# Kernel optimization log

Measured on AMD Instinct MI355X. Metric: run time of the kernel, lower is better.

The kernel has to match this reference:

```python
import jax, jax.numpy as jnp
import numpy as np

N = 50000      # nodes per type (tx and addr)
E = 400000     # edges per relation
IN, H, OUT = 128, 256, 2
RELS = ['tt', 'aa', 'at', 'ta']


def setup_inputs() -> dict:
    key = jax.random.key(0)
    ks = jax.random.split(key, 32)
    inp = {}
    inp['x_tx'] = jax.random.normal(ks[0], (N, IN), jnp.float32)
    inp['x_addr'] = jax.random.normal(ks[1], (N, IN), jnp.float32)
    for i, r in enumerate(RELS):
        inp['e_' + r] = jax.random.randint(ks[2 + i], (2, E), 0, N, jnp.int32)
    k = 6
    for li, (din, dout) in enumerate([(IN, H), (H, OUT)]):
        for r in RELS:
            inp[f'Wl{li}_{r}'] = jax.random.normal(ks[k], (dout, din), jnp.float32) * 0.05; k += 1
            inp[f'bl{li}_{r}'] = jnp.zeros((dout,), jnp.float32)
            inp[f'Wr{li}_{r}'] = jax.random.normal(ks[k], (dout, din), jnp.float32) * 0.05; k += 1
    return inp


def _sage(x_src, x_dst, edge, Wl, bl, Wr):
    # PyG SAGEConv: lin_l(mean_{j in N(i)} x_j) + lin_r(x_i)
    n = x_dst.shape[0]
    msg = x_src[edge[0]]                                         # [E, d] gather
    s = jax.ops.segment_sum(msg, edge[1], num_segments=n)        # [n, d] scatter-add
    cnt = jax.ops.segment_sum(jnp.ones((edge.shape[1],), x_src.dtype), edge[1], num_segments=n)
    agg = s / jnp.maximum(cnt, 1.0)[:, None]                     # mean (0 for isolated)
    return agg @ Wl.T + bl + x_dst @ Wr.T


def reference(x_tx, x_addr, e_tt, e_aa, e_at, e_ta,
              Wl0_tt, bl0_tt, Wr0_tt, Wl0_aa, bl0_aa, Wr0_aa,
              Wl0_at, bl0_at, Wr0_at, Wl0_ta, bl0_ta, Wr0_ta,
              Wl1_tt, bl1_tt, Wr1_tt, Wl1_aa, bl1_aa, Wr1_aa,
              Wl1_at, bl1_at, Wr1_at, Wl1_ta, bl1_ta, Wr1_ta):
    # Layer 0: HeteroConv with aggr='sum' over relations per destination type
    h_tx = _sage(x_tx, x_tx, e_tt, Wl0_tt, bl0_tt, Wr0_tt) + \
           _sage(x_addr, x_tx, e_at, Wl0_at, bl0_at, Wr0_at)
    h_ad = _sage(x_addr, x_addr, e_aa, Wl0_aa, bl0_aa, Wr0_aa) + \
           _sage(x_tx, x_addr, e_ta, Wl0_ta, bl0_ta, Wr0_ta)
    h_tx = jax.nn.relu(h_tx)   # dropout is identity at inference
    h_ad = jax.nn.relu(h_ad)
    # Layer 1 (output)
    o_tx = _sage(h_tx, h_tx, e_tt, Wl1_tt, bl1_tt, Wr1_tt) + \
           _sage(h_ad, h_tx, e_at, Wl1_at, bl1_at, Wr1_at)
    o_ad = _sage(h_ad, h_ad, e_aa, Wl1_aa, bl1_aa, Wr1_aa) + \
           _sage(h_tx, h_ad, e_ta, Wl1_ta, bl1_ta, Wr1_ta)
    return o_tx, o_ad
```

## Files before the change

kernel.cpp:

```cpp
#include <hip/hip_runtime.h>
#include <hip/hip_fp8.h>


#define DIN 128
#define DH  256
#define LDSA 136
#define LDSH 264

typedef __attribute__((ext_vector_type(8))) short bf16x8;
typedef __attribute__((ext_vector_type(4))) float f32x4;
typedef __attribute__((ext_vector_type(2))) float f32x2;

__device__ __forceinline__ float blo(unsigned u) { return __uint_as_float(u << 16); }
__device__ __forceinline__ float bhi(unsigned u) { return __uint_as_float(u & 0xffff0000u); }
__device__ __forceinline__ unsigned short f2bf(float f) {
    unsigned int u = __float_as_uint(f);
    u = (u + 0x7fffu + ((u >> 16) & 1u)) >> 16;
    return (unsigned short)u;
}

#if __has_builtin(__builtin_amdgcn_cvt_pk_fp8_f32) && __has_builtin(__builtin_amdgcn_cvt_pk_f32_fp8)
__device__ __forceinline__ unsigned pk_fp8(float4 a) {
    unsigned v = (unsigned)__builtin_amdgcn_cvt_pk_fp8_f32(a.x, a.y, 0, false);
    v = (unsigned)__builtin_amdgcn_cvt_pk_fp8_f32(a.z, a.w, (int)v, true);
    return v;
}
__device__ __forceinline__ void acc_fp8x4(float* a, unsigned u) {
    f32x2 f0 = __builtin_amdgcn_cvt_pk_f32_fp8((int)u, false);
    f32x2 f1 = __builtin_amdgcn_cvt_pk_f32_fp8((int)u, true);
    a[0] += f0.x; a[1] += f0.y; a[2] += f1.x; a[3] += f1.y;
}
#else
__device__ __forceinline__ unsigned pk_fp8(float4 a) {
    __hip_fp8_e4m3 v0(a.x), v1(a.y), v2(a.z), v3(a.w);
    return (unsigned)v0.__x | ((unsigned)v1.__x << 8) |
           ((unsigned)v2.__x << 16) | ((unsigned)v3.__x << 24);
}
__device__ __forceinline__ void acc_fp8x4(float* a, unsigned u) {
    __hip_fp8_e4m3 v0, v1, v2, v3;
    v0.__x = (unsigned char)(u & 0xff);
    v1.__x = (unsigned char)((u >> 8) & 0xff);
    v2.__x = (unsigned char)((u >> 16) & 0xff);
    v3.__x = (unsigned char)((u >> 24) & 0xff);
    a[0] += (float)v0; a[1] += (float)v1; a[2] += (float)v2; a[3] += (float)v3;
}
#endif

__device__ __forceinline__ void acc_fp8x16(float* a, uint4 u) {
    acc_fp8x4(a + 0,  u.x);
    acc_fp8x4(a + 4,  u.y);
    acc_fp8x4(a + 8,  u.z);
    acc_fp8x4(a + 12, u.w);
}

__global__ __launch_bounds__(256) void setup_kernel(
    const float* __restrict__ x_tx, const float* __restrict__ x_addr,
    const float* __restrict__ Wl0_tt, const float* __restrict__ Wl0_aa,
    const float* __restrict__ Wl0_at, const float* __restrict__ Wl0_ta,
    const float* __restrict__ Wr0_tt, const float* __restrict__ Wr0_aa,
    const float* __restrict__ Wr0_at, const float* __restrict__ Wr0_ta,
    const float* __restrict__ bl0_tt, const float* __restrict__ bl0_aa,
    const float* __restrict__ bl0_at, const float* __restrict__ bl0_ta,
    const float* __restrict__ Wl1_tt, const float* __restrict__ Wl1_aa,
    const float* __restrict__ Wl1_at, const float* __restrict__ Wl1_ta,
    const float* __restrict__ Wr1_tt, const float* __restrict__ Wr1_aa,
    const float* __restrict__ Wr1_at, const float* __restrict__ Wr1_ta,
    const float* __restrict__ bl1_tt, const float* __restrict__ bl1_aa,
    const float* __restrict__ bl1_at, const float* __restrict__ bl1_ta,
    unsigned short* __restrict__ xb_tx, unsigned short* __restrict__ xb_ad,
    uint2* __restrict__ x8_tx, uint2* __restrict__ x8_ad,
    unsigned short* __restrict__ wb_tt, unsigned short* __restrict__ wb_aa,
    unsigned short* __restrict__ wb_at, unsigned short* __restrict__ wb_ta,
    unsigned short* __restrict__ wr0c_tx, unsigned short* __restrict__ wr0c_ad,
    float* __restrict__ b0c, unsigned short* __restrict__ wzb,
    float* __restrict__ b1c, int N)
{
    int i = blockIdx.x * blockDim.x + threadIdx.x;
    int nconv = N * DIN / 8;
    if (i < nconv) {
        {
            const float4* p = (const float4*)(x_tx + (size_t)i * 8);
            float4 a = p[0], b = p[1];
            uint4 o;
            o.x = (unsigned)f2bf(a.x) | ((unsigned)f2bf(a.y) << 16);
            o.y = (unsigned)f2bf(a.z) | ((unsigned)f2bf(a.w) << 16);
            o.z = (unsigned)f2bf(b.x) | ((unsigned)f2bf(b.y) << 16);
            o.w = (unsigned)f2bf(b.z) | ((unsigned)f2bf(b.w) << 16);
            *(uint4*)(xb_tx + (size_t)i * 8) = o;
            x8_tx[i] = make_uint2(pk_fp8(a), pk_fp8(b));
        }
        {
            const float4* p = (const float4*)(x_addr + (size_t)i * 8);
            float4 a = p[0], b = p[1];
            uint4 o;
            o.x = (unsigned)f2bf(a.x) | ((unsigned)f2bf(a.y) << 16);
            o.y = (unsigned)f2bf(a.z) | ((unsigned)f2bf(a.w) << 16);
            o.z = (unsigned)f2bf(b.x) | ((unsigned)f2bf(b.y) << 16);
            o.w = (unsigned)f2bf(b.z) | ((unsigned)f2bf(b.w) << 16);
            *(uint4*)(xb_ad + (size_t)i * 8) = o;
            x8_ad[i] = make_uint2(pk_fp8(a), pk_fp8(b));
        }
    }
    if (i < DH * DIN) {
        wb_tt[i] = f2bf(Wl0_tt[i]);
        wb_aa[i] = f2bf(Wl0_aa[i]);
        wb_at[i] = f2bf(Wl0_at[i]);
        wb_ta[i] = f2bf(Wl0_ta[i]);
        wr0c_tx[i] = f2bf(Wr0_tt[i] + Wr0_at[i]);
        wr0c_ad[i] = f2bf(Wr0_aa[i] + Wr0_ta[i]);
    }
    if (i < DH) {
        b0c[i]      = bl0_tt[i] + bl0_at[i];
        b0c[DH + i] = bl0_aa[i] + bl0_ta[i];
    }
    if (i < 2 * 16 * DH) {
        int type = i >> 12;
        int rem = i & 4095;
        int r = rem >> 8;
        int c = rem & 255;
        float v = 0.f;
        if (r < 6) {
            const float* A = type ? Wl1_aa : Wl1_tt;
            const float* B = type ? Wl1_at : Wl1_ta;
            if (r == 0) v = A[c];
            else if (r == 1) v = A[DH + c];
            else if (r == 2) v = B[c];
            else if (r == 3) v = B[DH + c];
            else if (r == 4) v = type ? (Wr1_aa[c] + Wr1_ta[c]) : (Wr1_tt[c] + Wr1_at[c]);
            else             v = type ? (Wr1_aa[DH + c] + Wr1_ta[DH + c])
                                      : (Wr1_tt[DH + c] + Wr1_at[DH + c]);
        }
        wzb[i] = f2bf(v);
    }
    if (i < 2) {
        b1c[i]     = bl1_tt[i] + bl1_at[i];
        b1c[2 + i] = bl1_aa[i] + bl1_ta[i];
    }
}

__global__ __launch_bounds__(256) void count_kernel(
    const int* __restrict__ e0, const int* __restrict__ e1,
    const int* __restrict__ e2, const int* __restrict__ e3,
    int* __restrict__ cnt, int* __restrict__ rank, int E, int N)
{
    int r = blockIdx.y;
    const int* e = (r == 0) ? e0 : (r == 1) ? e1 : (r == 2) ? e2 : e3;
    int base = (blockIdx.x * 256 + threadIdx.x) * 8;
    int* cb = cnt + r * N;
    int* rk = rank + (size_t)r * E;
    if (base + 8 <= E) {
        int4 d0 = *(const int4*)(e + E + base);
        int4 d1 = *(const int4*)(e + E + base + 4);
        int4 r0, r1;
        r0.x = atomicAdd(&cb[d0.x], 1);
        r0.y = atomicAdd(&cb[d0.y], 1);
        r0.z = atomicAdd(&cb[d0.z], 1);
        r0.w = atomicAdd(&cb[d0.w], 1);
        r1.x = atomicAdd(&cb[d1.x], 1);
        r1.y = atomicAdd(&cb[d1.y], 1);
        r1.z = atomicAdd(&cb[d1.z], 1);
        r1.w = atomicAdd(&cb[d1.w], 1);
        *(int4*)(rk + base) = r0;
        *(int4*)(rk + base + 4) = r1;
    } else {
        for (int i = base; i < E; ++i)
            rk[i] = atomicAdd(&cb[e[E + i]], 1);
    }
}

__global__ __launch_bounds__(1024) void scan_kernel(
    const int* __restrict__ cnt, int* __restrict__ excl,
    unsigned long long* __restrict__ desc, int n)
{
    __shared__ int sdata[1024];
    __shared__ int sseg;
    __shared__ int sprev;
    if (threadIdx.x == 0) sseg = (int)atomicAdd(&desc[256], 1ULL);
    __syncthreads();
    int seg = sseg;
    int i = seg * 1024 + threadIdx.x;
    int v = (i < n) ? cnt[i] : 0;
    sdata[threadIdx.x] = v;
    __syncthreads();
    for (int off = 1; off < 1024; off <<= 1) {
        int t = (threadIdx.x >= off) ? sdata[threadIdx.x - off] : 0;
        __syncthreads();
        sdata[threadIdx.x] += t;
        __syncthreads();
    }
    if (threadIdx.x == 0) {
        int total = sdata[1023];
        int prev = 0;
        if (seg == 0) {
            atomicExch(&desc[0], ((unsigned long long)(unsigned)total << 2) | 2ULL);
        } else {
            atomicExch(&desc[seg], ((unsigned long long)(unsigned)total << 2) | 1ULL);
            int j = seg - 1;
            for (;;) {
                unsigned long long d = atomicAdd(&desc[j], 0ULL);
                unsigned st = (unsigned)(d & 3ULL);
                if (st == 0u) continue;
                prev += (int)(d >> 2);
                if (st == 2u) break;
                --j;
            }
            atomicExch(&desc[seg],
                       ((unsigned long long)(unsigned)(prev + total) << 2) | 2ULL);
        }
        sprev = prev;
    }
    __syncthreads();
    if (i < n) excl[i] = sprev + sdata[threadIdx.x] - v;
}

__global__ __launch_bounds__(256) void fill_kernel(
    const int* __restrict__ e0, const int* __restrict__ e1,
    const int* __restrict__ e2, const int* __restrict__ e3,
    const int* __restrict__ rowptr, const int* __restrict__ rank,
    int* __restrict__ col, int E, int N)
{
    int r = blockIdx.y;
    const int* e = (r == 0) ? e0 : (r == 1) ? e1 : (r == 2) ? e2 : e3;
    const int* rp = rowptr + r * N;
    const int* rk = rank + (size_t)r * E;
    int base = (blockIdx.x * 256 + threadIdx.x) * 4;
    if (base + 4 <= E) {
        int4 s = *(const int4*)(e + base);
        int4 d = *(const int4*)(e + E + base);
        int4 rr = *(const int4*)(rk + base);
        int p0 = rp[d.x], p1 = rp[d.y], p2 = rp[d.z], p3 = rp[d.w];
        col[p0 + rr.x] = s.x;
        col[p1 + rr.y] = s.y;
        col[p2 + rr.z] = s.z;
        col[p3 + rr.w] = s.w;
    } else {
        for (int i = base; i < E; ++i)
            col[rp[e[E + i]] + rk[i]] = e[i];
    }
}

__global__ __launch_bounds__(256) void agg_kernel(
    const uint4* __restrict__ x8_tx, const uint4* __restrict__ x8_ad,
    const int* __restrict__ rowptr, const int* __restrict__ cnt,
    const int* __restrict__ col, unsigned short* __restrict__ aggb, int N)
{
    int r = blockIdx.y;
    const uint4* xs = (r == 0 || r == 3) ? x8_tx : x8_ad;
    int t = threadIdx.x;
    int wv = t >> 6;
    int l  = t & 63;
    int oct = l >> 3;
    int d   = l & 7;
    int node = blockIdx.x * 32 + wv * 8 + oct;
    if (node >= N) return;
    int idx = r * N + node;
    int base = rowptr[idx];
    int c    = cnt[idx];
    const int* cl = col + base;
    float a0[16] = {}, a1[16] = {};
    int e = 0;
    for (; e + 2 <= c; e += 2) {
        int s0 = cl[e];
        int s1 = cl[e + 1];
        uint4 u0 = xs[((unsigned)s0 << 3) + d];
        uint4 u1 = xs[((unsigned)s1 << 3) + d];
        acc_fp8x16(a0, u0);
        acc_fp8x16(a1, u1);
    }
    if (e < c) {
        int s0 = cl[e];
        uint4 u0 = xs[((unsigned)s0 << 3) + d];
        acc_fp8x16(a0, u0);
    }
    float sc = 1.0f / fmaxf((float)c, 1.0f);
    uint4 o0, o1;
    o0.x = (unsigned)f2bf((a0[0] + a1[0]) * sc)  | ((unsigned)f2bf((a0[1] + a1[1]) * sc) << 16);
    o0.y = (unsigned)f2bf((a0[2] + a1[2]) * sc)  | ((unsigned)f2bf((a0[3] + a1[3]) * sc) << 16);
    o0.z = (unsigned)f2bf((a0[4] + a1[4]) * sc)  | ((unsigned)f2bf((a0[5] + a1[5]) * sc) << 16);
    o0.w = (unsigned)f2bf((a0[6] + a1[6]) * sc)  | ((unsigned)f2bf((a0[7] + a1[7]) * sc) << 16);
    o1.x = (unsigned)f2bf((a0[8] + a1[8]) * sc)  | ((unsigned)f2bf((a0[9] + a1[9]) * sc) << 16);
    o1.y = (unsigned)f2bf((a0[10] + a1[10]) * sc) | ((unsigned)f2bf((a0[11] + a1[11]) * sc) << 16);
    o1.z = (unsigned)f2bf((a0[12] + a1[12]) * sc) | ((unsigned)f2bf((a0[13] + a1[13]) * sc) << 16);
    o1.w = (unsigned)f2bf((a0[14] + a1[14]) * sc) | ((unsigned)f2bf((a0[15] + a1[15]) * sc) << 16);
    uint4* orow = (uint4*)(aggb + ((size_t)r * N + node) * DIN);
    orow[d * 2]     = o0;
    orow[d * 2 + 1] = o1;
}

__global__ __launch_bounds__(256) void gemm0z_kernel(
    const unsigned short* __restrict__ xb_tx, const unsigned short* __restrict__ xb_ad,
    const unsigned short* __restrict__ aggb,
    const unsigned short* __restrict__ wb_tt, const unsigned short* __restrict__ wb_at,
    const unsigned short* __restrict__ wr0c_tx,
    const unsigned short* __restrict__ wb_aa, const unsigned short* __restrict__ wb_ta,
    const unsigned short* __restrict__ wr0c_ad,
    const float* __restrict__ b0c, const unsigned short* __restrict__ wzb,
    const float* __restrict__ b1c,
    float* __restrict__ z, float* __restrict__ outp, int N)
{
    __shared__ unsigned short lds[3 * 64 * LDSA];
    const int type = blockIdx.y;
    const unsigned short* xself = type ? xb_ad : xb_tx;
    const unsigned short* A0 = aggb + (size_t)(type ? 1 : 0) * N * DIN;
    const unsigned short* A1 = aggb + (size_t)(type ? 3 : 2) * N * DIN;
    const unsigned short* W0 = type ? wb_aa   : wb_tt;
    const unsigned short* W1 = type ? wb_ta   : wb_at;
    const unsigned short* W2 = type ? wr0c_ad : wr0c_tx;
    const float* bias = b0c + type * DH;
    float* zA = type ? (z + (size_t)1 * N * 2) : z;
    float* zB = type ? (z + (size_t)2 * N * 2) : (z + (size_t)3 * N * 2);
    float* outSelf = outp + (size_t)type * N * 2;

    const int t  = threadIdx.x;
    const int wv = t >> 6;
    const int l  = t & 63;
    const int q  = l >> 4;
    const int lr = l & 15;
    const int m0 = blockIdx.x * 64;
    const int n0 = wv * 64;

    {
        const uint4* As[3] = {(const uint4*)A0, (const uint4*)A1, (const uint4*)xself};
#pragma unroll
        for (int i = 0; i < 12; ++i) {
            int cid = i * 256 + t;
            int seg = cid >> 10;
            int rem = cid & 1023;
            int row = rem >> 4;
            int ch  = rem & 15;
            int gr = m0 + row; if (gr >= N) gr = N - 1;
            uint4 v = As[seg][((unsigned)gr << 4) + ch];
            *(uint4*)&lds[(seg * 64 + row) * LDSA + ch * 8] = v;
        }
    }
    __syncthreads();

    f32x4 accm[4][4] = {};
    {
        const unsigned short* Ws[3] = {W0, W1, W2};
        for (int seg = 0; seg < 3; ++seg) {
            const unsigned short* W = Ws[seg];
            const unsigned short* la = &lds[(seg * 64 + lr) * LDSA + q * 8];
            const unsigned short* pb0 = W + (unsigned)(n0 + lr) * DIN + q * 8;
            const unsigned short* pb1 = W + (unsigned)(n0 + 16 + lr) * DIN + q * 8;
            const unsigned short* pb2 = W + (unsigned)(n0 + 32 + lr) * DIN + q * 8;
            const unsigned short* pb3 = W + (unsigned)(n0 + 48 + lr) * DIN + q * 8;
#pragma unroll
            for (int k = 0; k < DIN; k += 32) {
                bf16x8 b0 = *(const bf16x8*)(pb0 + k);
                bf16x8 b1 = *(const bf16x8*)(pb1 + k);
                bf16x8 b2 = *(const bf16x8*)(pb2 + k);
                bf16x8 b3 = *(const bf16x8*)(pb3 + k);
#pragma unroll
                for (int mt = 0; mt < 4; ++mt) {
                    bf16x8 a = *(const bf16x8*)(la + mt * 16 * LDSA + k);
                    accm[mt][0] = __builtin_amdgcn_mfma_f32_16x16x32_bf16(a, b0, accm[mt][0], 0, 0, 0);
                    accm[mt][1] = __builtin_amdgcn_mfma_f32_16x16x32_bf16(a, b1, accm[mt][1], 0, 0, 0);
                    accm[mt][2] = __builtin_amdgcn_mfma_f32_16x16x32_bf16(a, b2, accm[mt][2], 0, 0, 0);
                    accm[mt][3] = __builtin_amdgcn_mfma_f32_16x16x32_bf16(a, b3, accm[mt][3], 0, 0, 0);
                }
            }
        }
    }
    __syncthreads();

    {
        float bias_nt[4];
#pragma unroll
        for (int nt = 0; nt < 4; ++nt) bias_nt[nt] = bias[n0 + nt * 16 + lr];
#pragma unroll
        for (int mt = 0; mt < 4; ++mt) {
#pragma unroll
            for (int nt = 0; nt < 4; ++nt) {
                int colc = n0 + nt * 16 + lr;
#pragma unroll
                for (int rr = 0; rr < 4; ++rr) {
                    int row = mt * 16 + q * 4 + rr;
                    lds[row * LDSH + colc] =
                        f2bf(fmaxf(accm[mt][nt][rr] + bias_nt[nt], 0.f));
                }
            }
        }
    }
    __syncthreads();

    {
        const unsigned short* wz = wzb + (size_t)type * 16 * DH;
        f32x4 az = {};
        const unsigned short* la = &lds[(wv * 16 + lr) * LDSH + q * 8];
        const unsigned short* pb = wz + lr * DH + q * 8;
#pragma unroll
        for (int k = 0; k < DH; k += 32) {
            bf16x8 a = *(const bf16x8*)(la + k);
            bf16x8 b = *(const bf16x8*)(pb + k);
            az = __builtin_amdgcn_mfma_f32_16x16x32_bf16(a, b, az, 0, 0, 0);
        }
        if (lr < 6) {
#pragma unroll
            for (int reg = 0; reg < 4; ++reg) {
                int node = m0 + wv * 16 + q * 4 + reg;
                if (node < N) {
                    float v = az[reg];
                    if (lr < 2)      zA[node * 2 + lr] = v;
                    else if (lr < 4) zB[node * 2 + lr - 2] = v;
                    else             outSelf[node * 2 + lr - 4] = v + b1c[type * 2 + lr - 4];
                }
            }
        }
    }
}

__global__ __launch_bounds__(256) void l1_agg_kernel(
    const int* __restrict__ rowptr, const int* __restrict__ cnt, const int* __restrict__ col,
    const float* __restrict__ z, float* __restrict__ out, int N)
{
    const int type = blockIdx.y;
    const int rA = type ? 1 : 0;
    const int rB = type ? 3 : 2;
    const float* zAp = type ? (z + (size_t)1 * N * 2) : z;
    const float* zBp = type ? (z + (size_t)3 * N * 2) : (z + (size_t)2 * N * 2);
    float* outp = out + (size_t)type * N * 2;

    const int t = threadIdx.x;
    const int wave = t >> 6;
    const int l = t & 63;
    const int sub = l >> 3;
    const int es  = l & 7;
    int node = blockIdx.x * 32 + wave * 8 + sub;
    bool valid = node < N;

    float ax = 0.f, ay = 0.f;
#pragma unroll
    for (int ri = 0; ri < 2; ++ri) {
        int rel = ri ? rB : rA;
        const float* zp = ri ? zBp : zAp;
        int b = 0, c = 0;
        if (valid) { b = rowptr[rel * N + node]; c = cnt[rel * N + node]; }
        const int* cl = col + b;
        float sx = 0.f, sy = 0.f;
        for (int e = es; e < c; e += 8) {
            int s = cl[e];
            float2 v = *(const float2*)(zp + (size_t)s * 2);
            sx += v.x; sy += v.y;
        }
        sx += __shfl_xor(sx, 1, 64); sy += __shfl_xor(sy, 1, 64);
        sx += __shfl_xor(sx, 2, 64); sy += __shfl_xor(sy, 2, 64);
        sx += __shfl_xor(sx, 4, 64); sy += __shfl_xor(sy, 4, 64);
        float sc = 1.0f / fmaxf((float)c, 1.0f);
        ax += sx * sc; ay += sy * sc;
    }
    if (valid && es == 0) {
        float2 o = *(float2*)(outp + (size_t)node * 2);
        o.x += ax; o.y += ay;
        *(float2*)(outp + (size_t)node * 2) = o;
    }
}

extern "C" void kernel_launch(void* const* d_in, const int* in_sizes, int n_in,
                              void* d_out, int out_size, void* d_ws, size_t ws_size,
                              hipStream_t stream)
{
    const float* x_tx   = (const float*)d_in[0];
    const float* x_addr = (const float*)d_in[1];
    const int* e_tt = (const int*)d_in[2];
    const int* e_aa = (const int*)d_in[3];
    const int* e_at = (const int*)d_in[4];
    const int* e_ta = (const int*)d_in[5];
    const float* Wl0_tt = (const float*)d_in[6];
    const float* bl0_tt = (const float*)d_in[7];
    const float* Wr0_tt = (const float*)d_in[8];
    const float* Wl0_aa = (const float*)d_in[9];
    const float* bl0_aa = (const float*)d_in[10];
    const float* Wr0_aa = (const float*)d_in[11];
    const float* Wl0_at = (const float*)d_in[12];
    const float* bl0_at = (const float*)d_in[13];
    const float* Wr0_at = (const float*)d_in[14];
    const float* Wl0_ta = (const float*)d_in[15];
    const float* bl0_ta = (const float*)d_in[16];
    const float* Wr0_ta = (const float*)d_in[17];
    const float* Wl1_tt = (const float*)d_in[18];
    const float* bl1_tt = (const float*)d_in[19];
    const float* Wr1_tt = (const float*)d_in[20];
    const float* Wl1_aa = (const float*)d_in[21];
    const float* bl1_aa = (const float*)d_in[22];
    const float* Wr1_aa = (const float*)d_in[23];
    const float* Wl1_at = (const float*)d_in[24];
    const float* bl1_at = (const float*)d_in[25];
    const float* Wr1_at = (const float*)d_in[26];
    const float* Wl1_ta = (const float*)d_in[27];
    const float* bl1_ta = (const float*)d_in[28];
    const float* Wr1_ta = (const float*)d_in[29];

    const int N = in_sizes[0] / DIN;
    const int E = in_sizes[2] / 2;

    size_t off = 0;
    char* base = (char*)d_ws;
    auto alloc = [&](size_t bytes) -> void* {
        void* p = base + off;
        off += (bytes + 255) & ~(size_t)255;
        return p;
    };
    int*   cnt    = (int*)  alloc((size_t)4 * N * 4);
    unsigned long long* desc = (unsigned long long*)alloc(257 * 8);
    int*   rowptr = (int*)  alloc((size_t)4 * N * 4);
    int*   rank   = (int*)  alloc((size_t)4 * E * 4);
    int*   col    = (int*)  alloc((size_t)4 * E * 4);
    unsigned short* xb_tx = (unsigned short*)alloc((size_t)N * DIN * 2);
    unsigned short* xb_ad = (unsigned short*)alloc((size_t)N * DIN * 2);
    uint2* x8_tx = (uint2*)alloc((size_t)N * DIN);
    uint2* x8_ad = (uint2*)alloc((size_t)N * DIN);
    unsigned short* aggb  = (unsigned short*)alloc((size_t)4 * N * DIN * 2);
    float* z      = (float*)alloc((size_t)4 * N * 2 * 4);
    unsigned short* wb_tt  = (unsigned short*)alloc((size_t)DH * DIN * 2);
    unsigned short* wb_aa  = (unsigned short*)alloc((size_t)DH * DIN * 2);
    unsigned short* wb_at  = (unsigned short*)alloc((size_t)DH * DIN * 2);
    unsigned short* wb_ta  = (unsigned short*)alloc((size_t)DH * DIN * 2);
    unsigned short* wr0c_tx = (unsigned short*)alloc((size_t)DH * DIN * 2);
    unsigned short* wr0c_ad = (unsigned short*)alloc((size_t)DH * DIN * 2);
    float* b0c    = (float*)alloc((size_t)2 * DH * 4);
    unsigned short* wzb = (unsigned short*)alloc((size_t)2 * 16 * DH * 2);
    float* b1c    = (float*)alloc((size_t)2 * 2 * 4);
    (void)ws_size;

    float* outp = (float*)d_out;
    const int n4 = 4 * N;

    hipMemsetAsync(cnt, 0, (((size_t)4 * N * 4 + 255) & ~(size_t)255) + 257 * 8, stream);

    {
        int nconv = N * DIN / 8;
        setup_kernel<<<(nconv + 255) / 256, 256, 0, stream>>>(
            x_tx, x_addr,
            Wl0_tt, Wl0_aa, Wl0_at, Wl0_ta,
            Wr0_tt, Wr0_aa, Wr0_at, Wr0_ta,
            bl0_tt, bl0_aa, bl0_at, bl0_ta,
            Wl1_tt, Wl1_aa, Wl1_at, Wl1_ta,
            Wr1_tt, Wr1_aa, Wr1_at, Wr1_ta,
            bl1_tt, bl1_aa, bl1_at, bl1_ta,
            xb_tx, xb_ad, x8_tx, x8_ad,
            wb_tt, wb_aa, wb_at, wb_ta, wr0c_tx, wr0c_ad,
            b0c, wzb, b1c, N);
    }
    {
        dim3 g((E + 2047) / 2048, 4);
        count_kernel<<<g, 256, 0, stream>>>(e_tt, e_aa, e_at, e_ta, cnt, rank, E, N);
    }
    {
        int nb = (n4 + 1023) / 1024;
        scan_kernel<<<nb, 1024, 0, stream>>>(cnt, rowptr, desc, n4);
    }
    {
        dim3 g((E + 1023) / 1024, 4);
        fill_kernel<<<g, 256, 0, stream>>>(e_tt, e_aa, e_at, e_ta, rowptr, rank, col, E, N);
    }
    {
        dim3 g((N + 31) / 32, 4);
        agg_kernel<<<g, 256, 0, stream>>>((const uint4*)x8_tx, (const uint4*)x8_ad,
                                          rowptr, cnt, col, aggb, N);
    }
    {
        dim3 g((N + 63) / 64, 2);
        gemm0z_kernel<<<g, 256, 0, stream>>>(
            xb_tx, xb_ad, aggb,
            wb_tt, wb_at, wr0c_tx, wb_aa, wb_ta, wr0c_ad,
            b0c, wzb, b1c, z, outp, N);
    }
    {
        dim3 g((N + 31) / 32, 2);
        l1_agg_kernel<<<g, 256, 0, stream>>>(rowptr, cnt, col, z, outp, N);
    }
}
```

Baseline: 375.3 us.

## Build CSR via two-level bucket sort with LDS histograms instead of global atomics

Replaces the per-edge global atomic counting, decoupled-lookback scan and random fill with a two-pass bucket sort. Edges are first grouped into coarse buckets of 256 destinations using shared-memory histograms and one global atomic per bucket per block. A per-bucket kernel then sorts within the bucket in LDS and writes rowptr, cnt and col. This cuts global atomic contention and random scattered writes. The costs are an extra temp buffer pass, source ids packed into 16 bits (valid only for N ≤ 65536), and non-deterministic edge order within a row.

```diff
diff --git a/kernel.cpp b/kernel.cpp
--- a/kernel.cpp
+++ b/kernel.cpp
@@ -11,8 +11,6 @@
 typedef __attribute__((ext_vector_type(4))) float f32x4;
 typedef __attribute__((ext_vector_type(2))) float f32x2;
 
-__device__ __forceinline__ float blo(unsigned u) { return __uint_as_float(u << 16); }
-__device__ __forceinline__ float bhi(unsigned u) { return __uint_as_float(u & 0xffff0000u); }
 __device__ __forceinline__ unsigned short f2bf(float f) {
     unsigned int u = __float_as_uint(f);
     u = (u + 0x7fffu + ((u >> 16) & 1u)) >> 16;
@@ -138,104 +136,151 @@
     }
 }
 
-__global__ __launch_bounds__(256) void count_kernel(
+__global__ __launch_bounds__(256) void bhist_kernel(
     const int* __restrict__ e0, const int* __restrict__ e1,
     const int* __restrict__ e2, const int* __restrict__ e3,
-    int* __restrict__ cnt, int* __restrict__ rank, int E, int N)
+    int* __restrict__ bcnt, int E, int nb)
 {
     int r = blockIdx.y;
     const int* e = (r == 0) ? e0 : (r == 1) ? e1 : (r == 2) ? e2 : e3;
-    int base = (blockIdx.x * 256 + threadIdx.x) * 8;
-    int* cb = cnt + r * N;
-    int* rk = rank + (size_t)r * E;
-    if (base + 8 <= E) {
-        int4 d0 = *(const int4*)(e + E + base);
-        int4 d1 = *(const int4*)(e + E + base + 4);
-        int4 r0, r1;
-        r0.x = atomicAdd(&cb[d0.x], 1);
-        r0.y = atomicAdd(&cb[d0.y], 1);
-        r0.z = atomicAdd(&cb[d0.z], 1);
-        r0.w = atomicAdd(&cb[d0.w], 1);
-        r1.x = atomicAdd(&cb[d1.x], 1);
-        r1.y = atomicAdd(&cb[d1.y], 1);
-        r1.z = atomicAdd(&cb[d1.z], 1);
-        r1.w = atomicAdd(&cb[d1.w], 1);
-        *(int4*)(rk + base) = r0;
-        *(int4*)(rk + base + 4) = r1;
+    __shared__ int h[256];
+    if (threadIdx.x < nb) h[threadIdx.x] = 0;
+    __syncthreads();
+    int base = (blockIdx.x * 256 + threadIdx.x) * 16;
+    if (base + 16 <= E) {
+        const int4* p = (const int4*)(e + E + base);
+        int4 d0 = p[0], d1 = p[1], d2 = p[2], d3 = p[3];
+        atomicAdd(&h[(unsigned)d0.x >> 8], 1); atomicAdd(&h[(unsigned)d0.y >> 8], 1);
+        atomicAdd(&h[(unsigned)d0.z >> 8], 1); atomicAdd(&h[(unsigned)d0.w >> 8], 1);
+        atomicAdd(&h[(unsigned)d1.x >> 8], 1); atomicAdd(&h[(unsigned)d1.y >> 8], 1);
+        atomicAdd(&h[(unsigned)d1.z >> 8], 1); atomicAdd(&h[(unsigned)d1.w >> 8], 1);
+        atomicAdd(&h[(unsigned)d2.x >> 8], 1); atomicAdd(&h[(unsigned)d2.y >> 8], 1);
+        atomicAdd(&h[(unsigned)d2.z >> 8], 1); atomicAdd(&h[(unsigned)d2.w >> 8], 1);
+        atomicAdd(&h[(unsigned)d3.x >> 8], 1); atomicAdd(&h[(unsigned)d3.y >> 8], 1);
+        atomicAdd(&h[(unsigned)d3.z >> 8], 1); atomicAdd(&h[(unsigned)d3.w >> 8], 1);
     } else {
         for (int i = base; i < E; ++i)
-            rk[i] = atomicAdd(&cb[e[E + i]], 1);
-    }
-}
-
-__global__ __launch_bounds__(1024) void scan_kernel(
-    const int* __restrict__ cnt, int* __restrict__ excl,
-    unsigned long long* __restrict__ desc, int n)
-{
-    __shared__ int sdata[1024];
-    __shared__ int sseg;
-    __shared__ int sprev;
-    if (threadIdx.x == 0) sseg = (int)atomicAdd(&desc[256], 1ULL);
-    __syncthreads();
-    int seg = sseg;
-    int i = seg * 1024 + threadIdx.x;
-    int v = (i < n) ? cnt[i] : 0;
-    sdata[threadIdx.x] = v;
+            atomicAdd(&h[(unsigned)e[E + i] >> 8], 1);
+    }
+    __syncthreads();
+    if (threadIdx.x < nb) {
+        int v = h[threadIdx.x];
+        if (v) atomicAdd(&bcnt[r * nb + threadIdx.x], v);
+    }
+}
+
+__global__ __launch_bounds__(1024) void bscan_kernel(
+    const int* __restrict__ bcnt, int* __restrict__ bbase, int* __restrict__ bcur, int n)
+{
+    __shared__ int s[1024];
+    int t = threadIdx.x;
+    int v = (t < n) ? bcnt[t] : 0;
+    s[t] = v;
     __syncthreads();
     for (int off = 1; off < 1024; off <<= 1) {
-        int t = (threadIdx.x >= off) ? sdata[threadIdx.x - off] : 0;
+        int x = (t >= off) ? s[t - off] : 0;
         __syncthreads();
-        sdata[threadIdx.x] += t;
+        s[t] += x;
         __syncthreads();
     }
-    if (threadIdx.x == 0) {
-        int total = sdata[1023];
-        int prev = 0;
-        if (seg == 0) {
-            atomicExch(&desc[0], ((unsigned long long)(unsigned)total << 2) | 2ULL);
-        } else {
-            atomicExch(&desc[seg], ((unsigned long long)(unsigned)total << 2) | 1ULL);
-            int j = seg - 1;
-            for (;;) {
-                unsigned long long d = atomicAdd(&desc[j], 0ULL);
-                unsigned st = (unsigned)(d & 3ULL);
-                if (st == 0u) continue;
-                prev += (int)(d >> 2);
-                if (st == 2u) break;
-                --j;
-            }
-            atomicExch(&desc[seg],
-                       ((unsigned long long)(unsigned)(prev + total) << 2) | 2ULL);
-        }
-        sprev = prev;
-    }
-    __syncthreads();
-    if (i < n) excl[i] = sprev + sdata[threadIdx.x] - v;
-}
-
-__global__ __launch_bounds__(256) void fill_kernel(
+    if (t < n) {
+        int ex = s[t] - v;
+        bbase[t] = ex;
+        bcur[t] = ex;
+    }
+    if (t == 0) bbase[n] = s[1023];
+}
+
+__global__ __launch_bounds__(256) void bscatter_kernel(
     const int* __restrict__ e0, const int* __restrict__ e1,
     const int* __restrict__ e2, const int* __restrict__ e3,
-    const int* __restrict__ rowptr, const int* __restrict__ rank,
-    int* __restrict__ col, int E, int N)
+    int* __restrict__ bcur, unsigned* __restrict__ tmp, int E, int nb)
 {
     int r = blockIdx.y;
     const int* e = (r == 0) ? e0 : (r == 1) ? e1 : (r == 2) ? e2 : e3;
-    const int* rp = rowptr + r * N;
-    const int* rk = rank + (size_t)r * E;
-    int base = (blockIdx.x * 256 + threadIdx.x) * 4;
-    if (base + 4 <= E) {
-        int4 s = *(const int4*)(e + base);
-        int4 d = *(const int4*)(e + E + base);
-        int4 rr = *(const int4*)(rk + base);
-        int p0 = rp[d.x], p1 = rp[d.y], p2 = rp[d.z], p3 = rp[d.w];
-        col[p0 + rr.x] = s.x;
-        col[p1 + rr.y] = s.y;
-        col[p2 + rr.z] = s.z;
-        col[p3 + rr.w] = s.w;
+    __shared__ int h[256];
+    __shared__ int lbase[256];
+    __shared__ int lcur[256];
+    if (threadIdx.x < nb) { h[threadIdx.x] = 0; lcur[threadIdx.x] = 0; }
+    __syncthreads();
+    int base = (blockIdx.x * 256 + threadIdx.x) * 16;
+    int dst[16], src[16];
+    int cnt16 = 0;
+    if (base + 16 <= E) {
+        const int4* pd = (const int4*)(e + E + base);
+        const int4* ps = (const int4*)(e + base);
+#pragma unroll
+        for (int j = 0; j < 4; ++j) {
+            int4 d = pd[j], s4 = ps[j];
+            dst[j * 4 + 0] = d.x; dst[j * 4 + 1] = d.y; dst[j * 4 + 2] = d.z; dst[j * 4 + 3] = d.w;
+            src[j * 4 + 0] = s4.x; src[j * 4 + 1] = s4.y; src[j * 4 + 2] = s4.z; src[j * 4 + 3] = s4.w;
+        }
+        cnt16 = 16;
     } else {
-        for (int i = base; i < E; ++i)
-            col[rp[e[E + i]] + rk[i]] = e[i];
+        for (int i = base; i < E; ++i) {
+            dst[cnt16] = e[E + i];
+            src[cnt16] = e[i];
+            ++cnt16;
+        }
+    }
+    for (int j = 0; j < cnt16; ++j)
+        atomicAdd(&h[(unsigned)dst[j] >> 8], 1);
+    __syncthreads();
+    if (threadIdx.x < nb) {
+        int c = h[threadIdx.x];
+        if (c) lbase[threadIdx.x] = atomicAdd(&bcur[r * nb + threadIdx.x], c);
+    }
+    __syncthreads();
+    for (int j = 0; j < cnt16; ++j) {
+        int bk = (unsigned)dst[j] >> 8;
+        int rank = atomicAdd(&lcur[bk], 1);
+        tmp[lbase[bk] + rank] =
+            (((unsigned)dst[j] & 255u) << 16) | (unsigned)src[j];
+    }
+}
+
+__global__ __launch_bounds__(256) void bgroup_kernel(
+    const unsigned* __restrict__ tmp, const int* __restrict__ bbase,
+    int* __restrict__ col, int* __restrict__ rowptr, int* __restrict__ cnt,
+    int N, int nb)
+{
+    int b = blockIdx.x;
+    int r = blockIdx.y;
+    int idx = r * nb + b;
+    int lo = bbase[idx], hi = bbase[idx + 1];
+    __shared__ int h[256];
+    __shared__ int cur[256];
+    __shared__ int exs[256];
+    int t = threadIdx.x;
+    h[t] = 0; cur[t] = 0;
+    __syncthreads();
+    for (int i = lo + t; i < hi; i += 256)
+        atomicAdd(&h[(tmp[i] >> 16) & 255u], 1);
+    __syncthreads();
+    {
+        __shared__ int s[256];
+        int v = h[t];
+        s[t] = v;
+        __syncthreads();
+        for (int off = 1; off < 256; off <<= 1) {
+            int x = (t >= off) ? s[t - off] : 0;
+            __syncthreads();
+            s[t] += x;
+            __syncthreads();
+        }
+        exs[t] = s[t] - v;
+    }
+    __syncthreads();
+    int d = b * 256 + t;
+    if (d < N) {
+        rowptr[r * N + d] = lo + exs[t];
+        cnt[r * N + d] = h[t];
+    }
+    for (int i = lo + t; i < hi; i += 256) {
+        unsigned p = tmp[i];
+        int fine = (p >> 16) & 255u;
+        int rank = atomicAdd(&cur[fine], 1);
+        col[lo + exs[fine] + rank] = (int)(p & 0xffffu);
     }
 }
 
@@ -493,6 +538,7 @@
 
     const int N = in_sizes[0] / DIN;
     const int E = in_sizes[2] / 2;
+    const int nb = (N + 255) >> 8;
 
     size_t off = 0;
     char* base = (char*)d_ws;
@@ -501,11 +547,13 @@
         off += (bytes + 255) & ~(size_t)255;
         return p;
     };
+    int*   bcnt   = (int*)  alloc((size_t)4 * nb * 4);
+    int*   bbase  = (int*)  alloc(((size_t)4 * nb + 1) * 4);
+    int*   bcur   = (int*)  alloc((size_t)4 * nb * 4);
+    unsigned* tmp = (unsigned*)alloc((size_t)4 * E * 4);
+    int*   col    = (int*)  alloc((size_t)4 * E * 4);
+    int*   rowptr = (int*)  alloc((size_t)4 * N * 4);
     int*   cnt    = (int*)  alloc((size_t)4 * N * 4);
-    unsigned long long* desc = (unsigned long long*)alloc(257 * 8);
-    int*   rowptr = (int*)  alloc((size_t)4 * N * 4);
-    int*   rank   = (int*)  alloc((size_t)4 * E * 4);
-    int*   col    = (int*)  alloc((size_t)4 * E * 4);
     unsigned short* xb_tx = (unsigned short*)alloc((size_t)N * DIN * 2);
     unsigned short* xb_ad = (unsigned short*)alloc((size_t)N * DIN * 2);
     uint2* x8_tx = (uint2*)alloc((size_t)N * DIN);
@@ -524,9 +572,8 @@
     (void)ws_size;
 
     float* outp = (float*)d_out;
-    const int n4 = 4 * N;
-
-    hipMemsetAsync(cnt, 0, (((size_t)4 * N * 4 + 255) & ~(size_t)255) + 257 * 8, stream);
+
+    hipMemsetAsync(bcnt, 0, (size_t)4 * nb * 4, stream);
 
     {
         int nconv = N * DIN / 8;
@@ -543,16 +590,17 @@
             b0c, wzb, b1c, N);
     }
     {
-        dim3 g((E + 2047) / 2048, 4);
-        count_kernel<<<g, 256, 0, stream>>>(e_tt, e_aa, e_at, e_ta, cnt, rank, E, N);
-    }
-    {
-        int nb = (n4 + 1023) / 1024;
-        scan_kernel<<<nb, 1024, 0, stream>>>(cnt, rowptr, desc, n4);
-    }
-    {
-        dim3 g((E + 1023) / 1024, 4);
-        fill_kernel<<<g, 256, 0, stream>>>(e_tt, e_aa, e_at, e_ta, rowptr, rank, col, E, N);
+        dim3 g((E + 4095) / 4096, 4);
+        bhist_kernel<<<g, 256, 0, stream>>>(e_tt, e_aa, e_at, e_ta, bcnt, E, nb);
+    }
+    bscan_kernel<<<1, 1024, 0, stream>>>(bcnt, bbase, bcur, 4 * nb);
+    {
+        dim3 g((E + 4095) / 4096, 4);
+        bscatter_kernel<<<g, 256, 0, stream>>>(e_tt, e_aa, e_at, e_ta, bcur, tmp, E, nb);
+    }
+    {
+        dim3 g(nb, 4);
+        bgroup_kernel<<<g, 256, 0, stream>>>(tmp, bbase, col, rowptr, cnt, N, nb);
     }
     {
         dim3 g((N + 31) / 32, 4);
```

Result: faster. 303.2 us (-19.2%).
